# Kernel optimization log

Measured on AMD Instinct MI355X. Metric: run time of the kernel, lower is better.

Reference implementation:

```python
import jax, jax.numpy as jnp
import numpy as np

WS = 11          # window_size
SIGMA = 1.5
PAD = (WS - 1) // 2
C1 = (0.01 * 1.0) ** 2
C2 = (0.03 * 1.0) ** 2


def _gaussian_kernel2d():
    # kornia-style: 1D gaussian over window, normalized, outer product
    x = jnp.arange(WS, dtype=jnp.float32) - WS // 2
    g = jnp.exp(-(x ** 2) / (2.0 * SIGMA ** 2))
    g = g / jnp.sum(g)
    return jnp.outer(g, g)  # [WS, WS]


def _filter2d(x, k2d):
    # depthwise 2D filter with reflect ('same') padding, as kornia.filter2D
    b, c, h, w = x.shape
    xp = jnp.pad(x, ((0, 0), (0, 0), (PAD, PAD), (PAD, PAD)), mode='reflect')
    kern = jnp.broadcast_to(k2d.astype(x.dtype), (c, 1, WS, WS))
    return jax.lax.conv_general_dilated(
        xp, kern, window_strides=(1, 1), padding='VALID',
        feature_group_count=c,
        dimension_numbers=('NCHW', 'OIHW', 'NCHW'))


def setup_inputs() -> dict:
    key = jax.random.key(0)
    k1, k2 = jax.random.split(key)
    inp = jax.random.normal(k1, (16, 1, 1024, 1024), dtype=jnp.float32)
    tgt = jax.random.uniform(k2, (16, 1, 1024, 1024), dtype=jnp.float32)
    return {"input": inp, "target": tgt}


def reference(input, target):
    k2d = _gaussian_kernel2d()
    img1 = jax.nn.sigmoid(input)  # logsigmoid(x).exp() == sigmoid(x)
    img2 = target

    mu1 = _filter2d(img1, k2d)
    mu2 = _filter2d(img2, k2d)
    mu1_sq = mu1 * mu1
    mu2_sq = mu2 * mu2
    mu1_mu2 = mu1 * mu2

    sigma1_sq = _filter2d(img1 * img1, k2d) - mu1_sq
    sigma2_sq = _filter2d(img2 * img2, k2d) - mu2_sq
    sigma12 = _filter2d(img1 * img2, k2d) - mu1_mu2

    ssim_map = ((2.0 * mu1_mu2 + C1) * (2.0 * sigma12 + C2)) / (
        (mu1_sq + mu2_sq + C1) * (sigma1_sq + sigma2_sq + C2))
    loss = jnp.clip(1.0 - ssim_map, 0.0, 1.0) / 2.0
    return jnp.mean(loss)  # reduction='mean'
```

## Files before the change

### kernel.cpp

```cpp
#include <hip/hip_runtime.h>
#include <math.h>


typedef __attribute__((ext_vector_type(2))) float f2;

#define H_IMG 1024
#define W_IMG 1024
#define N_IMG 16
#define TILE_W 256
#define TILE_H 64
#define PADR 5
#define LDS_S2 268

constexpr float GW[11] = {
    0.00102838f, 0.00759877f, 0.03600077f, 0.10936069f, 0.21300553f,
    0.26601172f,
    0.21300553f, 0.10936069f, 0.03600077f, 0.00759877f, 0.00102838f};

__device__ __forceinline__ int reflect_i(int i, int n) {
    i = (i < 0) ? -i : i;
    i = (i >= n) ? (2 * n - 2 - i) : i;
    return i;
}

__device__ __forceinline__ float fast_sigmoid(float x) {
    return __builtin_amdgcn_rcpf(1.0f + __expf(-x));
}

__device__ __forceinline__ void ssim_emit(
    f2 mu, f2 sq, float e12, float& loss_sum)
{
    const float mu1 = mu.x, mu2 = mu.y;
    const float mu1s = mu1 * mu1;
    const float mu2s = mu2 * mu2;
    const float mu12 = mu1 * mu2;
    const float s1  = sq.x - mu1s;
    const float s2  = sq.y - mu2s;
    const float s12 = e12  - mu12;
    const float C1 = 1e-4f, C2 = 9e-4f;
    const float num = (2.0f * mu12 + C1) * (2.0f * s12 + C2);
    const float den = (mu1s + mu2s + C1) * (s1 + s2 + C2);
    float l = 1.0f - num * __builtin_amdgcn_rcpf(den);
    l = fminf(fmaxf(l, 0.0f), 1.0f) * 0.5f;
    loss_sum += l;
}

template<int NR>
__device__ __forceinline__ void load_group(
    const float* __restrict__ A, const float* __restrict__ B,
    int y_start, int gb, int c0, int c1, int tid,
    float (&pa)[11], float (&pb)[11], float (&pa2)[11], float (&pb2)[11])
{
#pragma unroll
    for (int r = 0; r < NR; ++r) {
        const int yy = reflect_i(y_start + gb + r, H_IMG);
        const size_t ro = (size_t)yy * W_IMG;
        pa[r] = A[ro + c0];
        pb[r] = B[ro + c0];
        if (tid < 2 * PADR) {
            pa2[r] = A[ro + c1];
            pb2[r] = B[ro + c1];
        }
    }
}

template<int NR>
__device__ __forceinline__ void write_group(
    f2 (*__restrict__ buf)[LDS_S2], int tid,
    const float (&pa)[11], const float (&pb)[11],
    const float (&pa2)[11], const float (&pb2)[11])
{
#pragma unroll
    for (int r = 0; r < NR; ++r) {
        buf[r][tid] = (f2){fast_sigmoid(pa[r]), pb[r]};
        if (tid < 2 * PADR)
            buf[r][TILE_W + tid] = (f2){fast_sigmoid(pa2[r]), pb2[r]};
    }
}

template<int NR, bool GUARD>
__device__ __forceinline__ void process_group(
    const f2 (*__restrict__ buf)[LDS_S2], int tid,
    f2 (&vAB)[11], f2 (&vSQ)[11], float (&vX)[11], float& loss_sum)
{
#pragma unroll
    for (int r = 0; r < NR; ++r) {
        f2 hAB = (f2)(0.0f), hSQ = (f2)(0.0f);
        float hab = 0.0f;
#pragma unroll
        for (int k = 0; k < 11; ++k) {
            const f2 v   = buf[r][tid + k];
            const f2 wa2 = ((f2)(GW[k])) * v;
            hAB += wa2;
            hSQ  = __builtin_elementwise_fma(wa2, v, hSQ);
            hab  = fmaf(wa2.x, v.y, hab);
        }
#pragma unroll
        for (int j = 0; j < 11; ++j) {
            if (!(GUARD && j > r)) {
                const int s = (r - j + 22) % 11;
                const f2 w2 = (f2)(GW[j]);
                vAB[s] = __builtin_elementwise_fma(w2, hAB, vAB[s]);
                vSQ[s] = __builtin_elementwise_fma(w2, hSQ, vSQ[s]);
                vX[s]  = fmaf(GW[j], hab, vX[s]);
            }
        }
        if (!GUARD || r == 10) {
            const int s = (r + 1) % 11;
            ssim_emit(vAB[s], vSQ[s], vX[s], loss_sum);
            vAB[s] = (f2)(0.0f); vSQ[s] = (f2)(0.0f); vX[s] = 0.0f;
        }
    }
}

__global__ __launch_bounds__(256, 2) void ssim_main(
    const float* __restrict__ inp, const float* __restrict__ tgt,
    float* __restrict__ out)
{
    __shared__ f2 buf[11][LDS_S2];
    __shared__ float red[4];

    const int tid = threadIdx.x;
    const int blk = blockIdx.x;
    const int b   = blk >> 6;
    const int rem = blk & 63;
    const int cx  = rem & 3;
    const int ry  = rem >> 2;
    const int x0  = cx * TILE_W;
    const int y0  = ry * TILE_H;

    const float* __restrict__ A = inp + (size_t)b * (H_IMG * (size_t)W_IMG);
    const float* __restrict__ B = tgt + (size_t)b * (H_IMG * (size_t)W_IMG);

    const int c0 = reflect_i(x0 - PADR + tid, W_IMG);
    const int c1 = (tid < 2 * PADR) ? reflect_i(x0 + TILE_W - PADR + tid, W_IMG) : 0;

    f2 vAB[11], vSQ[11];
    float vX[11];
#pragma unroll
    for (int j = 0; j < 11; ++j) {
        vAB[j] = (f2)(0.0f); vSQ[j] = (f2)(0.0f); vX[j] = 0.0f;
    }
    float pa[11], pb[11], pa2[11], pb2[11];
    float loss_sum = 0.0f;

    const int y_start = y0 - PADR;

    load_group<11>(A, B, y_start, 0, c0, c1, tid, pa, pb, pa2, pb2);
    write_group<11>(buf, tid, pa, pb, pa2, pb2);
    load_group<11>(A, B, y_start, 11, c0, c1, tid, pa, pb, pa2, pb2);
    __syncthreads();
    process_group<11, true>(buf, tid, vAB, vSQ, vX, loss_sum);

#pragma unroll 1
    for (int g = 1; g <= 5; ++g) {
        __syncthreads();
        write_group<11>(buf, tid, pa, pb, pa2, pb2);
        if (g <= 4)
            load_group<11>(A, B, y_start, (g + 1) * 11, c0, c1, tid, pa, pb, pa2, pb2);
        else
            load_group<8>(A, B, y_start, 66, c0, c1, tid, pa, pb, pa2, pb2);
        __syncthreads();
        process_group<11, false>(buf, tid, vAB, vSQ, vX, loss_sum);
    }

    __syncthreads();
    write_group<8>(buf, tid, pa, pb, pa2, pb2);
    __syncthreads();
    process_group<8, false>(buf, tid, vAB, vSQ, vX, loss_sum);

#pragma unroll
    for (int off = 32; off > 0; off >>= 1)
        loss_sum += __shfl_down(loss_sum, off, 64);
    const int wave = tid >> 6;
    if ((tid & 63) == 0) red[wave] = loss_sum;
    __syncthreads();
    if (tid == 0) {
        const float s = red[0] + red[1] + red[2] + red[3];
        atomicAdd(out, s * (1.0f / ((float)N_IMG * H_IMG * W_IMG)));
    }
}

extern "C" void kernel_launch(void* const* d_in, const int* in_sizes, int n_in,
                              void* d_out, int out_size, void* d_ws, size_t ws_size,
                              hipStream_t stream) {
    const float* inp = (const float*)d_in[0];
    const float* tgt = (const float*)d_in[1];
    float* out = (float*)d_out;

    hipMemsetAsync(out, 0, sizeof(float), stream);

    const int grid = N_IMG * 4 * (H_IMG / TILE_H);
    ssim_main<<<grid, 256, 0, stream>>>(inp, tgt, out);
}
```

Baseline: 193.8 us.

## Drop register prefetch, pack vertical cross accumulator, raise occupancy to four blocks

Result: slower. 329.3 us (+69.9%).

```diff
diff --git a/kernel.cpp b/kernel.cpp
--- a/kernel.cpp
+++ b/kernel.cpp
@@ -46,42 +46,33 @@
 }
 
 template<int NR>
-__device__ __forceinline__ void load_group(
+__device__ __forceinline__ void stage_group(
     const float* __restrict__ A, const float* __restrict__ B,
     int y_start, int gb, int c0, int c1, int tid,
-    float (&pa)[11], float (&pb)[11], float (&pa2)[11], float (&pb2)[11])
+    f2 (*__restrict__ buf)[LDS_S2])
 {
-#pragma unroll
+#pragma unroll 2
     for (int r = 0; r < NR; ++r) {
         const int yy = reflect_i(y_start + gb + r, H_IMG);
-        const size_t ro = (size_t)yy * W_IMG;
-        pa[r] = A[ro + c0];
-        pb[r] = B[ro + c0];
-        if (tid < 2 * PADR) {
-            pa2[r] = A[ro + c1];
-            pb2[r] = B[ro + c1];
+        const size_t ro = (size_t)yy << 10;
+        const float a0 = A[ro + c0];
+        const float b0 = B[ro + c0];
+        float a1 = 0.0f, b1 = 0.0f;
+        const bool halo = (tid < 2 * PADR);
+        if (halo) {
+            a1 = A[ro + c1];
+            b1 = B[ro + c1];
         }
-    }
-}
-
-template<int NR>
-__device__ __forceinline__ void write_group(
-    f2 (*__restrict__ buf)[LDS_S2], int tid,
-    const float (&pa)[11], const float (&pb)[11],
-    const float (&pa2)[11], const float (&pb2)[11])
-{
-#pragma unroll
-    for (int r = 0; r < NR; ++r) {
-        buf[r][tid] = (f2){fast_sigmoid(pa[r]), pb[r]};
-        if (tid < 2 * PADR)
-            buf[r][TILE_W + tid] = (f2){fast_sigmoid(pa2[r]), pb2[r]};
+        buf[r][tid] = (f2){fast_sigmoid(a0), b0};
+        if (halo)
+            buf[r][TILE_W + tid] = (f2){fast_sigmoid(a1), b1};
     }
 }
 
 template<int NR, bool GUARD>
 __device__ __forceinline__ void process_group(
     const f2 (*__restrict__ buf)[LDS_S2], int tid,
-    f2 (&vAB)[11], f2 (&vSQ)[11], float (&vX)[11], float& loss_sum)
+    f2 (&vAB)[11], f2 (&vSQ)[11], f2 (&vXp)[6], float& loss_sum)
 {
 #pragma unroll
     for (int r = 0; r < NR; ++r) {
@@ -102,18 +93,32 @@
                 const f2 w2 = (f2)(GW[j]);
                 vAB[s] = __builtin_elementwise_fma(w2, hAB, vAB[s]);
                 vSQ[s] = __builtin_elementwise_fma(w2, hSQ, vSQ[s]);
-                vX[s]  = fmaf(GW[j], hab, vX[s]);
             }
+        }
+#pragma unroll
+        for (int p = 0; p < 6; ++p) {
+            const int s0 = 2 * p, s1 = 2 * p + 1;
+            const int j0 = (r - s0 + 22) % 11;
+            const int j1 = (s1 <= 10) ? ((r - s1 + 22) % 11) : 0;
+            float w0 = GW[j0];
+            float w1 = (s1 <= 10) ? GW[j1] : 0.0f;
+            if (GUARD && j0 > r) w0 = 0.0f;
+            if (GUARD && (s1 > 10 || j1 > r)) w1 = 0.0f;
+            if (w0 != 0.0f || w1 != 0.0f)
+                vXp[p] = __builtin_elementwise_fma(
+                    (f2){w0, w1}, (f2){hab, hab}, vXp[p]);
         }
         if (!GUARD || r == 10) {
             const int s = (r + 1) % 11;
-            ssim_emit(vAB[s], vSQ[s], vX[s], loss_sum);
-            vAB[s] = (f2)(0.0f); vSQ[s] = (f2)(0.0f); vX[s] = 0.0f;
+            const float e12 = (s & 1) ? vXp[s >> 1].y : vXp[s >> 1].x;
+            ssim_emit(vAB[s], vSQ[s], e12, loss_sum);
+            vAB[s] = (f2)(0.0f); vSQ[s] = (f2)(0.0f);
+            if (s & 1) vXp[s >> 1].y = 0.0f; else vXp[s >> 1].x = 0.0f;
         }
     }
 }
 
-__global__ __launch_bounds__(256, 2) void ssim_main(
+__global__ __launch_bounds__(256, 4) void ssim_main(
     const float* __restrict__ inp, const float* __restrict__ tgt,
     float* __restrict__ out)
 {
@@ -135,39 +140,33 @@
     const int c0 = reflect_i(x0 - PADR + tid, W_IMG);
     const int c1 = (tid < 2 * PADR) ? reflect_i(x0 + TILE_W - PADR + tid, W_IMG) : 0;
 
-    f2 vAB[11], vSQ[11];
-    float vX[11];
+    f2 vAB[11], vSQ[11], vXp[6];
 #pragma unroll
     for (int j = 0; j < 11; ++j) {
-        vAB[j] = (f2)(0.0f); vSQ[j] = (f2)(0.0f); vX[j] = 0.0f;
+        vAB[j] = (f2)(0.0f); vSQ[j] = (f2)(0.0f);
     }
-    float pa[11], pb[11], pa2[11], pb2[11];
+#pragma unroll
+    for (int p = 0; p < 6; ++p) vXp[p] = (f2)(0.0f);
     float loss_sum = 0.0f;
 
     const int y_start = y0 - PADR;
 
-    load_group<11>(A, B, y_start, 0, c0, c1, tid, pa, pb, pa2, pb2);
-    write_group<11>(buf, tid, pa, pb, pa2, pb2);
-    load_group<11>(A, B, y_start, 11, c0, c1, tid, pa, pb, pa2, pb2);
+    stage_group<11>(A, B, y_start, 0, c0, c1, tid, buf);
     __syncthreads();
-    process_group<11, true>(buf, tid, vAB, vSQ, vX, loss_sum);
+    process_group<11, true>(buf, tid, vAB, vSQ, vXp, loss_sum);
 
 #pragma unroll 1
     for (int g = 1; g <= 5; ++g) {
         __syncthreads();
-        write_group<11>(buf, tid, pa, pb, pa2, pb2);
-        if (g <= 4)
-            load_group<11>(A, B, y_start, (g + 1) * 11, c0, c1, tid, pa, pb, pa2, pb2);
-        else
-            load_group<8>(A, B, y_start, 66, c0, c1, tid, pa, pb, pa2, pb2);
+        stage_group<11>(A, B, y_start, g * 11, c0, c1, tid, buf);
         __syncthreads();
-        process_group<11, false>(buf, tid, vAB, vSQ, vX, loss_sum);
+        process_group<11, false>(buf, tid, vAB, vSQ, vXp, loss_sum);
     }
 
     __syncthreads();
-    write_group<8>(buf, tid, pa, pb, pa2, pb2);
+    stage_group<8>(A, B, y_start, 66, c0, c1, tid, buf);
     __syncthreads();
-    process_group<8, false>(buf, tid, vAB, vSQ, vX, loss_sum);
+    process_group<8, false>(buf, tid, vAB, vSQ, vXp, loss_sum);
 
 #pragma unroll
     for (int off = 32; off > 0; off >>= 1)
```
